# Kernel optimization log

Hardware: AMD Instinct MI355X
Metric: run time of the kernel (lower is better)

Reference implementation:

```python
import jax, jax.numpy as jnp
import numpy as np

B, S, D, H, DH = 2, 2048, 768, 12, 64
ROT, BASE, WIN = 64, 10000.0, 128
SCALE = float(np.sqrt(DH))  # cfg.attn_scale = sqrt(d_head) = 8.0


def _sin_cos():
    # TransformerLens calculate_sin_cos_rotary, rotary_adjacent_pairs=False
    pos = jnp.arange(S, dtype=jnp.float32)
    freq = BASE ** (jnp.arange(0, ROT, 2, dtype=jnp.float32) / ROT)
    freq = jnp.concatenate([freq, freq])  # 'd -> (2 d)'
    angles = pos[:, None] / freq[None, :]  # [S, ROT]
    return jnp.sin(angles), jnp.cos(angles)


def _rotate_every_two(v):
    n = v.shape[-1] // 2
    return jnp.concatenate([-v[..., n:], v[..., :n]], axis=-1)


def _apply_rotary(x, sin, cos):
    # x: [B, S, H, DH]; rotate first ROT dims, pass rest through
    xr, xp = x[..., :ROT], x[..., ROT:]
    c = cos[None, :, None, :]
    s = sin[None, :, None, :]
    return jnp.concatenate([xr * c + _rotate_every_two(xr) * s, xp], axis=-1)


def setup_inputs() -> dict:
    key = jax.random.key(0)
    ks = jax.random.split(key, 7)
    init = lambda k, shape: jax.random.normal(k, shape, jnp.float32) / np.sqrt(D).astype(np.float32)
    return dict(
        query_input=jax.random.normal(ks[0], (B, S, D), jnp.float32),
        key_input=jax.random.normal(ks[1], (B, S, D), jnp.float32),
        value_input=jax.random.normal(ks[2], (B, S, D), jnp.float32),
        W_Q=init(ks[3], (H, D, DH)),
        W_K=init(ks[4], (H, D, DH)),
        W_V=init(ks[5], (H, D, DH)),
        W_O=init(ks[6], (H, DH, D)),
        b_Q=jnp.zeros((H, DH), jnp.float32),
        b_K=jnp.zeros((H, DH), jnp.float32),
        b_V=jnp.zeros((H, DH), jnp.float32),
        b_O=jnp.zeros((D,), jnp.float32),
    )


def reference(query_input, key_input, value_input, W_Q, W_K, W_V, W_O, b_Q, b_K, b_V, b_O):
    # QKV projections (calculate_qkv_matrices)
    q = jnp.einsum('bpd,hdk->bphk', query_input, W_Q) + b_Q
    k = jnp.einsum('bpd,hdk->bphk', key_input, W_K) + b_K
    v = jnp.einsum('bpd,hdk->bphk', value_input, W_V) + b_V
    # rotary (kv_cache_pos_offset = 0)
    sin, cos = _sin_cos()
    q = _apply_rotary(q, sin, cos)
    k = _apply_rotary(k, sin, cos)
    # attention scores
    scores = jnp.einsum('bqhd,bkhd->bhqk', q, k) / SCALE
    # position_bias defaults to zeros -> no-op
    i = jnp.arange(S)[:, None]
    j = jnp.arange(S)[None, :]
    mask = (j <= i) & (j > i - WIN)
    scores = jnp.where(mask[None, None], scores, -jnp.inf)
    pattern = jax.nn.softmax(scores, axis=-1)
    pattern = jnp.where(jnp.isnan(pattern), 0.0, pattern)
    z = jnp.einsum('bhqk,bkhd->bqhd', pattern, v)  # [B, S, H, DH]
    # output projection: z flattened @ W_O (rearranged) + b_O
    out = z.reshape(B, S, H * DH) @ W_O.reshape(H * DH, D) + b_O
    return out
```

## Files before the change

kernel.cpp:

```cpp
#include <hip/hip_runtime.h>
#include <hip/hip_bf16.h>

#define BB 2
#define SS 2048
#define DD 768
#define HH 12
#define DHH 64
#define WIN 128
#define MM (BB*SS)

typedef __attribute__((ext_vector_type(8))) short bfrag;
typedef __attribute__((ext_vector_type(4))) float f32x4;
typedef __attribute__((ext_vector_type(4))) short s16x4;

#define AS3(p) ((__attribute__((address_space(3))) void*)(p))
#define AS1(p) ((const __attribute__((address_space(1))) void*)(p))

__device__ inline unsigned short f2bf(float f) {
    union { __hip_bfloat16 h; unsigned short u; } cv;
    cv.h = __float2bfloat16(f);
    return cv.u;
}

__device__ inline void stage128(unsigned short* dst, const unsigned short* src,
                                int w4, int l) {
    #pragma unroll
    for (int j = 0; j < 2; j++) {
        int eoff = (w4 * 2 + j) * 512;
        int e = eoff + l * 8;
        int row = e >> 5;
        int k8 = ((e >> 3) & 3) ^ ((row >> 1) & 3);
        __builtin_amdgcn_global_load_lds(AS1(src + (size_t)row * DD + k8 * 8),
                                         AS3(dst + eoff), 16, 0, 0);
    }
}
__device__ inline void stage64(unsigned short* dst, const unsigned short* src,
                               int w4, int l) {
    int eoff = w4 * 512;
    int e = eoff + l * 8;
    int row = e >> 5;
    int k8 = ((e >> 3) & 3) ^ ((row >> 1) & 3);
    __builtin_amdgcn_global_load_lds(AS1(src + (size_t)row * DD + k8 * 8),
                                     AS3(dst + eoff), 16, 0, 0);
}

__global__ __launch_bounds__(256) void pack_kernel(
    const float* __restrict__ Xq, const float* __restrict__ Xk, const float* __restrict__ Xv,
    const float* __restrict__ Wq, const float* __restrict__ Wk, const float* __restrict__ Wv,
    const float* __restrict__ Wo,
    unsigned short* __restrict__ Wt, unsigned short* __restrict__ Wot,
    float2* __restrict__ rope, unsigned short* __restrict__ Xbf)
{
    __shared__ float T[64][65];
    const int bid = blockIdx.x, t = threadIdx.x;
    if (bid < 432) {
        int proj = bid / 144, rem = bid % 144;
        int h = rem / 12, d0 = (rem % 12) * 64;
        const float* src = (proj == 0 ? Wq : (proj == 1 ? Wk : Wv)) + (size_t)h * DD * DHH;
        int row = t >> 2, c0 = (t & 3) * 16;
        const float4* p4 = reinterpret_cast<const float4*>(src + (size_t)(d0 + row) * DHH + c0);
        float4 x0 = p4[0], x1 = p4[1], x2 = p4[2], x3 = p4[3];
        float* tr = &T[row][c0];
        tr[0]=x0.x; tr[1]=x0.y; tr[2]=x0.z; tr[3]=x0.w;
        tr[4]=x1.x; tr[5]=x1.y; tr[6]=x1.z; tr[7]=x1.w;
        tr[8]=x2.x; tr[9]=x2.y; tr[10]=x2.z; tr[11]=x2.w;
        tr[12]=x3.x; tr[13]=x3.y; tr[14]=x3.z; tr[15]=x3.w;
        __syncthreads();
        int dh = t >> 2;
        unsigned short tmp[16];
        #pragma unroll
        for (int j = 0; j < 16; j++) tmp[j] = f2bf(T[c0 + j][dh]);
        unsigned short* dst = Wt + (size_t)proj * DD * DD + (size_t)(h * 64 + dh) * DD + d0 + c0;
        *reinterpret_cast<bfrag*>(dst)     = *reinterpret_cast<bfrag*>(tmp);
        *reinterpret_cast<bfrag*>(dst + 8) = *reinterpret_cast<bfrag*>(tmp + 8);
    } else if (bid < 576) {
        int id2 = bid - 432;
        int k0 = (id2 / 12) * 64, n0 = (id2 % 12) * 64;
        int row = t >> 2, c0 = (t & 3) * 16;
        const float4* p4 = reinterpret_cast<const float4*>(Wo + (size_t)(k0 + row) * DD + n0 + c0);
        float4 x0 = p4[0], x1 = p4[1], x2 = p4[2], x3 = p4[3];
        float* tr = &T[row][c0];
        tr[0]=x0.x; tr[1]=x0.y; tr[2]=x0.z; tr[3]=x0.w;
        tr[4]=x1.x; tr[5]=x1.y; tr[6]=x1.z; tr[7]=x1.w;
        tr[8]=x2.x; tr[9]=x2.y; tr[10]=x2.z; tr[11]=x2.w;
        tr[12]=x3.x; tr[13]=x3.y; tr[14]=x3.z; tr[15]=x3.w;
        __syncthreads();
        int nr = t >> 2;
        unsigned short tmp[16];
        #pragma unroll
        for (int j = 0; j < 16; j++) tmp[j] = f2bf(T[c0 + j][nr]);
        unsigned short* dst = Wot + (size_t)(n0 + nr) * DD + k0 + c0;
        *reinterpret_cast<bfrag*>(dst)     = *reinterpret_cast<bfrag*>(tmp);
        *reinterpret_cast<bfrag*>(dst + 8) = *reinterpret_cast<bfrag*>(tmp + 8);
    } else if (bid < 832) {
        int idx = (bid - 576) * 256 + t;
        int p = idx >> 5, i2 = idx & 31;
        float inv_freq = exp2f(-(float)i2 * (13.287712379549449f / 32.0f));
        float s, c;
        sincosf((float)p * inv_freq, &s, &c);
        rope[idx] = make_float2(s, c);
    } else {
        int i = bid - 832;
        int proj = i / 768;
        size_t off = (size_t)(i % 768) * 4096 + t * 16;
        const float* src = (proj == 0 ? Xq : (proj == 1 ? Xk : Xv)) + off;
        const float4* p4 = reinterpret_cast<const float4*>(src);
        float4 a0 = p4[0], a1 = p4[1], a2 = p4[2], a3 = p4[3];
        unsigned short u[16];
        u[0]=f2bf(a0.x); u[1]=f2bf(a0.y); u[2]=f2bf(a0.z); u[3]=f2bf(a0.w);
        u[4]=f2bf(a1.x); u[5]=f2bf(a1.y); u[6]=f2bf(a1.z); u[7]=f2bf(a1.w);
        u[8]=f2bf(a2.x); u[9]=f2bf(a2.y); u[10]=f2bf(a2.z); u[11]=f2bf(a2.w);
        u[12]=f2bf(a3.x); u[13]=f2bf(a3.y); u[14]=f2bf(a3.z); u[15]=f2bf(a3.w);
        unsigned short* dst = Xbf + (size_t)proj * MM * DD + off;
        *reinterpret_cast<bfrag*>(dst)     = *reinterpret_cast<bfrag*>(u);
        *reinterpret_cast<bfrag*>(dst + 8) = *reinterpret_cast<bfrag*>(u + 8);
    }
}

__global__ __launch_bounds__(256) void qkv_gemm_kernel(
    const unsigned short* __restrict__ Xbf,
    const unsigned short* __restrict__ Wt,
    const float* __restrict__ bq, const float* __restrict__ bk, const float* __restrict__ bv,
    const float2* __restrict__ rope,
    unsigned short* __restrict__ qo, unsigned short* __restrict__ ko, unsigned short* __restrict__ vo)
{
    const int mt0  = blockIdx.x * 128;
    const int n0   = blockIdx.y * 128;
    const int proj = blockIdx.z;
    const unsigned short* X = Xbf + (size_t)proj * MM * DD + (size_t)mt0 * DD;
    const unsigned short* W = Wt + (size_t)proj * DD * DD + (size_t)n0 * DD;
    const float* bias = proj == 0 ? bq : (proj == 1 ? bk : bv);

    __shared__ unsigned short smem[3 * 8192];

    const int t = threadIdx.x;
    const int l = t & 63, w4 = t >> 6;
    const int l16 = l & 15, quad = l >> 4;
    const int wr = w4 >> 1, wc = w4 & 1;
    const int swz = (l16 >> 1) & 3;

    f32x4 acc[16] = {};

    stage128(smem,               X,      w4, l);
    stage128(smem + 4096,        W,      w4, l);
    stage128(smem + 8192,        X + 32, w4, l);
    stage128(smem + 8192 + 4096, W + 32, w4, l);

    for (int it = 0; it < 24; ++it) {
        unsigned short* Ac = smem + (it % 3) * 8192;
        unsigned short* Bc = Ac + 4096;
        if (it < 23) asm volatile("s_waitcnt vmcnt(4)" ::: "memory");
        else         asm volatile("s_waitcnt vmcnt(0)" ::: "memory");
        __builtin_amdgcn_s_barrier();
        if (it < 22) {
            unsigned short* An = smem + ((it + 2) % 3) * 8192;
            stage128(An,        X + (it + 2) * 32, w4, l);
            stage128(An + 4096, W + (it + 2) * 32, w4, l);
        }
        bfrag af[4], bg[4];
        #pragma unroll
        for (int mi = 0; mi < 4; mi++)
            af[mi] = *reinterpret_cast<const bfrag*>(&Ac[(wr * 64 + mi * 16 + l16) * 32 + ((quad ^ swz) * 8)]);
        #pragma unroll
        for (int ni = 0; ni < 4; ni++)
            bg[ni] = *reinterpret_cast<const bfrag*>(&Bc[(wc * 64 + ni * 16 + l16) * 32 + ((quad ^ swz) * 8)]);
        #pragma unroll
        for (int mi = 0; mi < 4; mi++)
            #pragma unroll
            for (int ni = 0; ni < 4; ni++)
                acc[mi * 4 + ni] = __builtin_amdgcn_mfma_f32_16x16x32_bf16(af[mi], bg[ni], acc[mi * 4 + ni], 0, 0, 0);
    }
    __syncthreads();

    unsigned short* Ct = smem;
    const int b = mt0 >> 11;
    if (proj < 2) {
        #pragma unroll
        for (int ni = 0; ni < 4; ni++) {
            int nloc = wc * 64 + ni * 16 + l16;
            int n = n0 + nloc;
            int dh = n & 63;
            float bv0 = bias[n];
            float bv1 = bias[n ^ 32];
            float sgn = (dh & 32) ? 1.0f : -1.0f;
            const float2* rp = rope + (dh & 31);
            #pragma unroll
            for (int mi = 0; mi < 4; mi++)
                #pragma unroll
                for (int r = 0; r < 4; r++) {
                    int ploc = wr * 64 + mi * 16 + quad * 4 + r;
                    int p = (mt0 + ploc) & (SS - 1);
                    float2 sc = rp[p << 5];
                    float val = acc[mi * 4 + ni][r] + bv0;
                    float pr  = acc[mi * 4 + (ni ^ 2)][r] + bv1;
                    Ct[ploc * 140 + nloc] = f2bf(val * sc.y + sgn * pr * sc.x);
                }
        }
        __syncthreads();
        unsigned short* dst = (proj == 0) ? qo : ko;
        #pragma unroll
        for (int jj = 0; jj < 8; jj++) {
            int id = jj * 256 + t;
            int row = id >> 4, c = (id & 15) * 8;
            int n = n0 + c, h = n >> 6, dh = n & 63;
            int p = (mt0 + row) & (SS - 1);
            bfrag vv = *reinterpret_cast<const bfrag*>(&Ct[row * 140 + c]);
            *reinterpret_cast<bfrag*>(dst + (((size_t)(b * HH + h) * SS + p) << 6) + dh) = vv;
        }
    } else {
        #pragma unroll
        for (int ni = 0; ni < 4; ni++) {
            int nloc = wc * 64 + ni * 16 + l16;
            float bv0 = bias[n0 + nloc];
            #pragma unroll
            for (int mi = 0; mi < 4; mi++)
                #pragma unroll
                for (int r = 0; r < 4; r++) {
                    int ploc = wr * 64 + mi * 16 + quad * 4 + r;
                    Ct[nloc * 140 + ploc] = f2bf(acc[mi * 4 + ni][r] + bv0);
                }
        }
        __syncthreads();
        int p0 = mt0 & (SS - 1);
        #pragma unroll
        for (int jj = 0; jj < 8; jj++) {
            int id = jj * 256 + t;
            int row = id >> 4, c = (id & 15) * 8;
            int n = n0 + row, h = n >> 6, dh = n & 63;
            bfrag vv = *reinterpret_cast<const bfrag*>(&Ct[row * 140 + c]);
            *reinterpret_cast<bfrag*>(vo + (((size_t)(b * HH + h) * DHH + dh) << 11) + p0 + c) = vv;
        }
    }
}

__global__ __launch_bounds__(256) void attn_kernel(
    const unsigned short* __restrict__ q,
    const unsigned short* __restrict__ k,
    const unsigned short* __restrict__ v,
    unsigned short* __restrict__ z)
{
    const int qb = blockIdx.x * 64;
    const int h  = blockIdx.y;
    const int b  = blockIdx.z;
    const int kb = qb - WIN;

    __shared__ unsigned short sA[25088];

    const int t = threadIdx.x;
    const int w4 = t >> 6, l = t & 63;
    const int l16 = l & 15, quad = l >> 4;
    const int swz = (l16 >> 1) & 3;

    const size_t qkbase = (size_t)(b * HH + h) * SS * DHH;
    const unsigned short* kp = (k + qkbase) + (ptrdiff_t)kb * DHH;
    const unsigned short* vp = (v + (size_t)(b * HH + h) * DHH * SS) + (ptrdiff_t)kb;

    #pragma unroll
    for (int j = 0; j < 6; j++) {
        int g = w4 * 6 + j;
        int panel = g >> 2, sub = g & 3;
        int rg = panel >> 1, kpart = panel & 1;
        int e = sub * 512 + l * 8;
        int row = e >> 5;
        int k8 = ((e >> 3) & 3) ^ ((row >> 1) & 3);
        __builtin_amdgcn_global_load_lds(
            AS1(kp + (size_t)(rg * 64 + row) * DHH + kpart * 32 + k8 * 8),
            AS3(sA + panel * 2048 + sub * 512), 16, 0, 0);
    }
    #pragma unroll
    for (int j = 0; j < 6; j++) {
        int g = w4 * 6 + j;
        int F = g * 64 + l;
        int d = F / 24, s = F % 24;
        int cs = s ^ (d & 7);
        __builtin_amdgcn_global_load_lds(
            AS1(vp + (size_t)d * SS + cs * 8),
            AS3(sA + 12800 + g * 512), 16, 0, 0);
    }
    bfrag qf[2];
    #pragma unroll
    for (int kk = 0; kk < 2; kk++)
        qf[kk] = *reinterpret_cast<const bfrag*>(
            q + qkbase + (size_t)(qb + 16 * w4 + l16) * DHH + kk * 32 + quad * 8);

    __syncthreads();

    f32x4 sacc[9] = {};
    __builtin_amdgcn_s_setprio(1);
    #pragma unroll
    for (int kk = 0; kk < 2; kk++)
        #pragma unroll
        for (int j = 0; j < 9; j++) {
            int kr = 16 * (w4 + j) + l16;
            bfrag bf = *reinterpret_cast<const bfrag*>(
                &sA[(((kr >> 6) * 2 + kk) * 2048) + (kr & 63) * 32 + ((quad ^ swz) * 8)]);
            sacc[j] = __builtin_amdgcn_mfma_f32_16x16x32_bf16(qf[kk], bf, sacc[j], 0, 0, 0);
        }
    __builtin_amdgcn_s_setprio(0);

    float mx[4] = {-3e38f, -3e38f, -3e38f, -3e38f};
    #pragma unroll
    for (int j = 0; j < 9; j++)
        #pragma unroll
        for (int r = 0; r < 4; r++) {
            int row = 16 * w4 + quad * 4 + r;
            int c = 16 * (w4 + j) + l16;
            bool valid = (c > row) && (c <= row + WIN) && (kb + c >= 0);
            float s = valid ? sacc[j][r] * 0.125f : -3e38f;
            sacc[j][r] = s;
            mx[r] = fmaxf(mx[r], s);
        }
    #pragma unroll
    for (int off = 1; off < 16; off <<= 1)
        #pragma unroll
        for (int r = 0; r < 4; r++) mx[r] = fmaxf(mx[r], __shfl_xor(mx[r], off, 64));
    float sum[4] = {0.f, 0.f, 0.f, 0.f};
    #pragma unroll
    for (int j = 0; j < 9; j++)
        #pragma unroll
        for (int r = 0; r < 4; r++) {
            float p = __expf(sacc[j][r] - mx[r]);
            sacc[j][r] = p;
            sum[r] += p;
        }
    #pragma unroll
    for (int off = 1; off < 16; off <<= 1)
        #pragma unroll
        for (int r = 0; r < 4; r++) sum[r] += __shfl_xor(sum[r], off, 64);
    float inv[4];
    #pragma unroll
    for (int r = 0; r < 4; r++) inv[r] = 1.0f / sum[r];

    __syncthreads();

    unsigned short* Ps = sA;
    #pragma unroll
    for (int j = 0; j < 9; j++)
        #pragma unroll
        for (int r = 0; r < 4; r++)
            Ps[(16 * w4 + quad * 4 + r) * 200 + 16 * (w4 + j) + l16] = f2bf(sacc[j][r] * inv[r]);
    {
        int mtz = (w4 & 1) ? (w4 - 1) : (w4 + 9);
        #pragma unroll
        for (int r = 0; r < 4; r++)
            Ps[(16 * w4 + quad * 4 + r) * 200 + 16 * mtz + l16] = 0;
    }

    unsigned short* Vt = sA + 12800;
    f32x4 zacc[4] = {};
    __builtin_amdgcn_s_setprio(1);
    #pragma unroll
    for (int ji = 0; ji < 5; ji++) {
        int ci = (w4 >> 1) + ji;
        bfrag pb = *reinterpret_cast<const bfrag*>(
            &Ps[(16 * w4 + l16) * 200 + ci * 32 + quad * 8]);
        #pragma unroll
        for (int mt = 0; mt < 4; mt++) {
            int d = 16 * mt + l16;
            bfrag va = *reinterpret_cast<const bfrag*>(
                &Vt[d * 192 + (((ci * 4 + quad) ^ (l16 & 7)) * 8)]);
            zacc[mt] = __builtin_amdgcn_mfma_f32_16x16x32_bf16(va, pb, zacc[mt], 0, 0, 0);
        }
    }
    __builtin_amdgcn_s_setprio(0);
    size_t zrow = ((size_t)(b * SS + qb + 16 * w4 + l16)) * (HH * DHH) + h * DHH;
    #pragma unroll
    for (int mt = 0; mt < 4; mt++) {
        s16x4 pk;
        pk[0] = (short)f2bf(zacc[mt][0]);
        pk[1] = (short)f2bf(zacc[mt][1]);
        pk[2] = (short)f2bf(zacc[mt][2]);
        pk[3] = (short)f2bf(zacc[mt][3]);
        *reinterpret_cast<s16x4*>(z + zrow + 16 * mt + quad * 4) = pk;
    }
}

__global__ __launch_bounds__(256) void out_gemm_kernel(
    const unsigned short* __restrict__ Z,
    const unsigned short* __restrict__ Wot,
    const float* __restrict__ bo,
    float* __restrict__ out)
{
    const int mt0 = blockIdx.x * 64;
    const int n0  = blockIdx.y * 64;
    const unsigned short* A = Z + (size_t)mt0 * DD;
    const unsigned short* Bw = Wot + (size_t)n0 * DD;

    __shared__ unsigned short smem[3 * 8192];

    const int t = threadIdx.x;
    const int l = t & 63, w4 = t >> 6;
    const int l16 = l & 15, quad = l >> 4;
    const int swz = (l16 >> 1) & 3;

    f32x4 acc[4] = {};

    #pragma unroll
    for (int s = 0; s < 2; s++) {
        unsigned short* sl = smem + s * 8192;
        stage64(sl,        A  + s * 64,      w4, l);
        stage64(sl + 2048, A  + s * 64 + 32, w4, l);
        stage64(sl + 4096, Bw + s * 64,      w4, l);
        stage64(sl + 6144, Bw + s * 64 + 32, w4, l);
    }

    for (int it = 0; it < 12; ++it) {
        unsigned short* Ac = smem + (it % 3) * 8192;
        unsigned short* Bc = Ac + 4096;
        if (it < 11) asm volatile("s_waitcnt vmcnt(4)" ::: "memory");
        else         asm volatile("s_waitcnt vmcnt(0)" ::: "memory");
        __builtin_amdgcn_s_barrier();
        if (it < 10) {
            unsigned short* An = smem + ((it + 2) % 3) * 8192;
            stage64(An,        A  + (it + 2) * 64,      w4, l);
            stage64(An + 2048, A  + (it + 2) * 64 + 32, w4, l);
            stage64(An + 4096, Bw + (it + 2) * 64,      w4, l);
            stage64(An + 6144, Bw + (it + 2) * 64 + 32, w4, l);
        }
        #pragma unroll
        for (int kk = 0; kk < 2; kk++) {
            bfrag af = *reinterpret_cast<const bfrag*>(
                &Ac[kk * 2048 + (w4 * 16 + l16) * 32 + ((quad ^ swz) * 8)]);
            #pragma unroll
            for (int ni = 0; ni < 4; ni++) {
                bfrag bg = *reinterpret_cast<const bfrag*>(
                    &Bc[kk * 2048 + (ni * 16 + l16) * 32 + ((quad ^ swz) * 8)]);
                acc[ni] = __builtin_amdgcn_mfma_f32_16x16x32_bf16(af, bg, acc[ni], 0, 0, 0);
            }
        }
    }

    #pragma unroll
    for (int ni = 0; ni < 4; ni++) {
        int n = n0 + ni * 16 + l16;
        float bv0 = bo[n];
        #pragma unroll
        for (int r = 0; r < 4; r++) {
            int m = mt0 + w4 * 16 + quad * 4 + r;
            out[(size_t)m * DD + n] = acc[ni][r] + bv0;
        }
    }
}

extern "C" void kernel_launch(void* const* d_in, const int* in_sizes, int n_in,
                              void* d_out, int out_size, void* d_ws, size_t ws_size,
                              hipStream_t stream) {
    const float* Xq = (const float*)d_in[0];
    const float* Xk = (const float*)d_in[1];
    const float* Xv = (const float*)d_in[2];
    const float* Wq = (const float*)d_in[3];
    const float* Wk = (const float*)d_in[4];
    const float* Wv = (const float*)d_in[5];
    const float* Wo = (const float*)d_in[6];
    const float* bq = (const float*)d_in[7];
    const float* bk = (const float*)d_in[8];
    const float* bv = (const float*)d_in[9];
    const float* bo = (const float*)d_in[10];
    float* out = (float*)d_out;

    const size_t seg = (size_t)BB * HH * SS * DHH;
    unsigned short* q   = (unsigned short*)d_ws;
    unsigned short* k   = q + seg;
    unsigned short* v   = k + seg;
    unsigned short* z   = v + seg;
    unsigned short* Wt  = z + seg;
    unsigned short* Wot = Wt + (size_t)3 * DD * DD;
    float2* rope = (float2*)(Wot + (size_t)DD * DD);
    unsigned short* Xbf = (unsigned short*)(rope + 2048 * 32);

    pack_kernel<<<dim3(3136), 256, 0, stream>>>(Xq, Xk, Xv, Wq, Wk, Wv, Wo, Wt, Wot, rope, Xbf);
    qkv_gemm_kernel<<<dim3(MM / 128, DD / 128, 3), 256, 0, stream>>>(
        Xbf, Wt, bq, bk, bv, rope, q, k, v);
    attn_kernel<<<dim3(SS / 64, HH, BB), 256, 0, stream>>>(q, k, v, z);
    out_gemm_kernel<<<dim3(MM / 64, DD / 64), 256, 0, stream>>>(z, Wot, bo, out);
}
```

Baseline: 162.6 us.

## Fuse output projection into attention kernel via per-row-block completion flags

```diff
diff --git a/kernel.cpp b/kernel.cpp
--- a/kernel.cpp
+++ b/kernel.cpp
@@ -49,7 +49,8 @@
     const float* __restrict__ Wq, const float* __restrict__ Wk, const float* __restrict__ Wv,
     const float* __restrict__ Wo,
     unsigned short* __restrict__ Wt, unsigned short* __restrict__ Wot,
-    float2* __restrict__ rope, unsigned short* __restrict__ Xbf)
+    float2* __restrict__ rope, unsigned short* __restrict__ Xbf,
+    unsigned int* __restrict__ flags)
 {
     __shared__ float T[64][65];
     const int bid = blockIdx.x, t = threadIdx.x;
@@ -93,6 +94,7 @@
         *reinterpret_cast<bfrag*>(dst)     = *reinterpret_cast<bfrag*>(tmp);
         *reinterpret_cast<bfrag*>(dst + 8) = *reinterpret_cast<bfrag*>(tmp + 8);
     } else if (bid < 832) {
+        if (bid == 576 && t < 64) flags[t] = 0u;
         int idx = (bid - 576) * 256 + t;
         int p = idx >> 5, i2 = idx & 31;
         float inv_freq = exp2f(-(float)i2 * (13.287712379549449f / 32.0f));
@@ -233,11 +235,15 @@
     }
 }
 
-__global__ __launch_bounds__(256) void attn_kernel(
+__global__ __launch_bounds__(256, 3) void attn_out_kernel(
     const unsigned short* __restrict__ q,
     const unsigned short* __restrict__ k,
     const unsigned short* __restrict__ v,
-    unsigned short* __restrict__ z)
+    unsigned short* __restrict__ z,
+    const unsigned short* __restrict__ Wot,
+    const float* __restrict__ bo,
+    float* __restrict__ out,
+    unsigned int* __restrict__ flags)
 {
     const int qb = blockIdx.x * 64;
     const int h  = blockIdx.y;
@@ -373,27 +379,28 @@
         pk[3] = (short)f2bf(zacc[mt][3]);
         *reinterpret_cast<s16x4*>(z + zrow + 16 * mt + quad * 4) = pk;
     }
-}
-
-__global__ __launch_bounds__(256) void out_gemm_kernel(
-    const unsigned short* __restrict__ Z,
-    const unsigned short* __restrict__ Wot,
-    const float* __restrict__ bo,
-    float* __restrict__ out)
-{
-    const int mt0 = blockIdx.x * 64;
-    const int n0  = blockIdx.y * 64;
-    const unsigned short* A = Z + (size_t)mt0 * DD;
+
+    __syncthreads();
+    if (t == 0)
+        __hip_atomic_fetch_add(&flags[b * 32 + blockIdx.x], 1u,
+                               __ATOMIC_RELEASE, __HIP_MEMORY_SCOPE_AGENT);
+
+    const int obid = blockIdx.x + 32 * (blockIdx.y + 12 * blockIdx.z);
+    const int om = obid & 63;
+    const int on = obid >> 6;
+    if (t == 0) {
+        while (__hip_atomic_load(&flags[om], __ATOMIC_ACQUIRE, __HIP_MEMORY_SCOPE_AGENT) < 12u)
+            __builtin_amdgcn_s_sleep(16);
+    }
+    __syncthreads();
+
+    const int mt0 = om * 64;
+    const int n0  = on * 64;
+    const unsigned short* A  = z + (size_t)mt0 * DD;
     const unsigned short* Bw = Wot + (size_t)n0 * DD;
-
-    __shared__ unsigned short smem[3 * 8192];
-
-    const int t = threadIdx.x;
-    const int l = t & 63, w4 = t >> 6;
-    const int l16 = l & 15, quad = l >> 4;
-    const int swz = (l16 >> 1) & 3;
-
-    f32x4 acc[4] = {};
+    unsigned short* smem = sA;
+
+    f32x4 oacc[4] = {};
 
     #pragma unroll
     for (int s = 0; s < 2; s++) {
@@ -425,7 +432,7 @@
             for (int ni = 0; ni < 4; ni++) {
                 bfrag bg = *reinterpret_cast<const bfrag*>(
                     &Bc[kk * 2048 + (ni * 16 + l16) * 32 + ((quad ^ swz) * 8)]);
-                acc[ni] = __builtin_amdgcn_mfma_f32_16x16x32_bf16(af, bg, acc[ni], 0, 0, 0);
+                oacc[ni] = __builtin_amdgcn_mfma_f32_16x16x32_bf16(af, bg, oacc[ni], 0, 0, 0);
             }
         }
     }
@@ -437,7 +444,7 @@
         #pragma unroll
         for (int r = 0; r < 4; r++) {
             int m = mt0 + w4 * 16 + quad * 4 + r;
-            out[(size_t)m * DD + n] = acc[ni][r] + bv0;
+            out[(size_t)m * DD + n] = oacc[ni][r] + bv0;
         }
     }
 }
@@ -467,10 +474,10 @@
     unsigned short* Wot = Wt + (size_t)3 * DD * DD;
     float2* rope = (float2*)(Wot + (size_t)DD * DD);
     unsigned short* Xbf = (unsigned short*)(rope + 2048 * 32);
-
-    pack_kernel<<<dim3(3136), 256, 0, stream>>>(Xq, Xk, Xv, Wq, Wk, Wv, Wo, Wt, Wot, rope, Xbf);
+    unsigned int* flags = (unsigned int*)(Xbf + (size_t)3 * MM * DD);
+
+    pack_kernel<<<dim3(3136), 256, 0, stream>>>(Xq, Xk, Xv, Wq, Wk, Wv, Wo, Wt, Wot, rope, Xbf, flags);
     qkv_gemm_kernel<<<dim3(MM / 128, DD / 128, 3), 256, 0, stream>>>(
         Xbf, Wt, bq, bk, bv, rope, q, k, v);
-    attn_kernel<<<dim3(SS / 64, HH, BB), 256, 0, stream>>>(q, k, v, z);
-    out_gemm_kernel<<<dim3(MM / 64, DD / 64), 256, 0, stream>>>(z, Wot, bo, out);
-}
+    attn_out_kernel<<<dim3(SS / 64, HH, BB), 256, 0, stream>>>(q, k, v, z, Wot, bo, out, flags);
+}
```

Result: slower. 213.7 us (+31.4%).

## Fuse fp32-to-bf16 activation conversion into QKV GEMM A-tile staging

Applied to the files above, without the earlier changes.

```diff
diff --git a/kernel.cpp b/kernel.cpp
--- a/kernel.cpp
+++ b/kernel.cpp
@@ -45,11 +45,10 @@
 }
 
 __global__ __launch_bounds__(256) void pack_kernel(
-    const float* __restrict__ Xq, const float* __restrict__ Xk, const float* __restrict__ Xv,
     const float* __restrict__ Wq, const float* __restrict__ Wk, const float* __restrict__ Wv,
     const float* __restrict__ Wo,
     unsigned short* __restrict__ Wt, unsigned short* __restrict__ Wot,
-    float2* __restrict__ rope, unsigned short* __restrict__ Xbf)
+    float2* __restrict__ rope)
 {
     __shared__ float T[64][65];
     const int bid = blockIdx.x, t = threadIdx.x;
@@ -92,33 +91,18 @@
         unsigned short* dst = Wot + (size_t)(n0 + nr) * DD + k0 + c0;
         *reinterpret_cast<bfrag*>(dst)     = *reinterpret_cast<bfrag*>(tmp);
         *reinterpret_cast<bfrag*>(dst + 8) = *reinterpret_cast<bfrag*>(tmp + 8);
-    } else if (bid < 832) {
+    } else {
         int idx = (bid - 576) * 256 + t;
         int p = idx >> 5, i2 = idx & 31;
         float inv_freq = exp2f(-(float)i2 * (13.287712379549449f / 32.0f));
         float s, c;
         sincosf((float)p * inv_freq, &s, &c);
         rope[idx] = make_float2(s, c);
-    } else {
-        int i = bid - 832;
-        int proj = i / 768;
-        size_t off = (size_t)(i % 768) * 4096 + t * 16;
-        const float* src = (proj == 0 ? Xq : (proj == 1 ? Xk : Xv)) + off;
-        const float4* p4 = reinterpret_cast<const float4*>(src);
-        float4 a0 = p4[0], a1 = p4[1], a2 = p4[2], a3 = p4[3];
-        unsigned short u[16];
-        u[0]=f2bf(a0.x); u[1]=f2bf(a0.y); u[2]=f2bf(a0.z); u[3]=f2bf(a0.w);
-        u[4]=f2bf(a1.x); u[5]=f2bf(a1.y); u[6]=f2bf(a1.z); u[7]=f2bf(a1.w);
-        u[8]=f2bf(a2.x); u[9]=f2bf(a2.y); u[10]=f2bf(a2.z); u[11]=f2bf(a2.w);
-        u[12]=f2bf(a3.x); u[13]=f2bf(a3.y); u[14]=f2bf(a3.z); u[15]=f2bf(a3.w);
-        unsigned short* dst = Xbf + (size_t)proj * MM * DD + off;
-        *reinterpret_cast<bfrag*>(dst)     = *reinterpret_cast<bfrag*>(u);
-        *reinterpret_cast<bfrag*>(dst + 8) = *reinterpret_cast<bfrag*>(u + 8);
     }
 }
 
 __global__ __launch_bounds__(256) void qkv_gemm_kernel(
-    const unsigned short* __restrict__ Xbf,
+    const float* __restrict__ Xq, const float* __restrict__ Xk, const float* __restrict__ Xv,
     const unsigned short* __restrict__ Wt,
     const float* __restrict__ bq, const float* __restrict__ bk, const float* __restrict__ bv,
     const float2* __restrict__ rope,
@@ -127,7 +111,7 @@
     const int mt0  = blockIdx.x * 128;
     const int n0   = blockIdx.y * 128;
     const int proj = blockIdx.z;
-    const unsigned short* X = Xbf + (size_t)proj * MM * DD + (size_t)mt0 * DD;
+    const float* Xa = (proj == 0 ? Xq : (proj == 1 ? Xk : Xv)) + (size_t)mt0 * DD;
     const unsigned short* W = Wt + (size_t)proj * DD * DD + (size_t)n0 * DD;
     const float* bias = proj == 0 ? bq : (proj == 1 ? bk : bv);
 
@@ -139,24 +123,46 @@
     const int wr = w4 >> 1, wc = w4 & 1;
     const int swz = (l16 >> 1) & 3;
 
+    const int arow = t >> 1, ahalf = t & 1;
+    const int swzr = (arow >> 1) & 3;
+    const size_t abase = (size_t)arow * DD + ahalf * 16;
+    const int aslot0 = ((2 * ahalf + 0) ^ swzr) * 8;
+    const int aslot1 = ((2 * ahalf + 1) ^ swzr) * 8;
+
     f32x4 acc[16] = {};
 
-    stage128(smem,               X,      w4, l);
+    #pragma unroll
+    for (int s = 0; s < 2; s++) {
+        const float4* ap = reinterpret_cast<const float4*>(Xa + abase + s * 32);
+        float4 f0 = ap[0], f1 = ap[1], f2 = ap[2], f3 = ap[3];
+        unsigned short u[16];
+        u[0]=f2bf(f0.x); u[1]=f2bf(f0.y); u[2]=f2bf(f0.z); u[3]=f2bf(f0.w);
+        u[4]=f2bf(f1.x); u[5]=f2bf(f1.y); u[6]=f2bf(f1.z); u[7]=f2bf(f1.w);
+        u[8]=f2bf(f2.x); u[9]=f2bf(f2.y); u[10]=f2bf(f2.z); u[11]=f2bf(f2.w);
+        u[12]=f2bf(f3.x); u[13]=f2bf(f3.y); u[14]=f2bf(f3.z); u[15]=f2bf(f3.w);
+        unsigned short* Ad = smem + s * 8192 + arow * 32;
+        *reinterpret_cast<bfrag*>(Ad + aslot0) = *reinterpret_cast<bfrag*>(u);
+        *reinterpret_cast<bfrag*>(Ad + aslot1) = *reinterpret_cast<bfrag*>(u + 8);
+    }
     stage128(smem + 4096,        W,      w4, l);
-    stage128(smem + 8192,        X + 32, w4, l);
     stage128(smem + 8192 + 4096, W + 32, w4, l);
 
     for (int it = 0; it < 24; ++it) {
         unsigned short* Ac = smem + (it % 3) * 8192;
         unsigned short* Bc = Ac + 4096;
-        if (it < 23) asm volatile("s_waitcnt vmcnt(4)" ::: "memory");
-        else         asm volatile("s_waitcnt vmcnt(0)" ::: "memory");
+        if (it < 23) asm volatile("s_waitcnt vmcnt(2) lgkmcnt(0)" ::: "memory");
+        else         asm volatile("s_waitcnt vmcnt(0) lgkmcnt(0)" ::: "memory");
         __builtin_amdgcn_s_barrier();
-        if (it < 22) {
-            unsigned short* An = smem + ((it + 2) % 3) * 8192;
-            stage128(An,        X + (it + 2) * 32, w4, l);
+
+        float4 f0, f1, f2, f3;
+        unsigned short* An = smem + ((it + 2) % 3) * 8192;
+        const bool st = (it < 22);
+        if (st) {
+            const float4* ap = reinterpret_cast<const float4*>(Xa + abase + (it + 2) * 32);
+            f0 = ap[0]; f1 = ap[1]; f2 = ap[2]; f3 = ap[3];
             stage128(An + 4096, W + (it + 2) * 32, w4, l);
         }
+
         bfrag af[4], bg[4];
         #pragma unroll
         for (int mi = 0; mi < 4; mi++)
@@ -169,6 +175,17 @@
             #pragma unroll
             for (int ni = 0; ni < 4; ni++)
                 acc[mi * 4 + ni] = __builtin_amdgcn_mfma_f32_16x16x32_bf16(af[mi], bg[ni], acc[mi * 4 + ni], 0, 0, 0);
+
+        if (st) {
+            unsigned short u[16];
+            u[0]=f2bf(f0.x); u[1]=f2bf(f0.y); u[2]=f2bf(f0.z); u[3]=f2bf(f0.w);
+            u[4]=f2bf(f1.x); u[5]=f2bf(f1.y); u[6]=f2bf(f1.z); u[7]=f2bf(f1.w);
+            u[8]=f2bf(f2.x); u[9]=f2bf(f2.y); u[10]=f2bf(f2.z); u[11]=f2bf(f2.w);
+            u[12]=f2bf(f3.x); u[13]=f2bf(f3.y); u[14]=f2bf(f3.z); u[15]=f2bf(f3.w);
+            unsigned short* Ad = An + arow * 32;
+            *reinterpret_cast<bfrag*>(Ad + aslot0) = *reinterpret_cast<bfrag*>(u);
+            *reinterpret_cast<bfrag*>(Ad + aslot1) = *reinterpret_cast<bfrag*>(u + 8);
+        }
     }
     __syncthreads();
 
@@ -466,11 +483,10 @@
     unsigned short* Wt  = z + seg;
     unsigned short* Wot = Wt + (size_t)3 * DD * DD;
     float2* rope = (float2*)(Wot + (size_t)DD * DD);
-    unsigned short* Xbf = (unsigned short*)(rope + 2048 * 32);
-
-    pack_kernel<<<dim3(3136), 256, 0, stream>>>(Xq, Xk, Xv, Wq, Wk, Wv, Wo, Wt, Wot, rope, Xbf);
+
+    pack_kernel<<<dim3(832), 256, 0, stream>>>(Wq, Wk, Wv, Wo, Wt, Wot, rope);
     qkv_gemm_kernel<<<dim3(MM / 128, DD / 128, 3), 256, 0, stream>>>(
-        Xbf, Wt, bq, bk, bv, rope, q, k, v);
+        Xq, Xk, Xv, Wt, bq, bk, bv, rope, q, k, v);
     attn_kernel<<<dim3(SS / 64, HH, BB), 256, 0, stream>>>(q, k, v, z);
     out_gemm_kernel<<<dim3(MM / 64, DD / 64), 256, 0, stream>>>(z, Wot, bo, out);
 }
```

After: 170.7 us. 4.9% more time.
